# Kernel optimization log

Measured on AMD Instinct MI355X. Metric: run time of the kernel, lower is better.

The kernel has to match this reference:

```python
import jax, jax.numpy as jnp
import numpy as np

NUM_LEVELS = 16
RESOLUTIONS = np.array([16, 18, 20, 22, 25, 27, 30, 34, 38, 42, 47, 52, 58, 64, 72, 80], dtype=np.int32)
OFFSETS = np.concatenate([np.zeros(1, np.int64), np.cumsum(RESOLUTIONS.astype(np.int64) ** 3)]).astype(np.int32)
BATCH = 2
C_IN = 16
C_OUT = 16
K = 3


def setup_inputs() -> dict:
    key = jax.random.key(0)
    k1, k2, k3 = jax.random.split(key, 3)
    n_total = int(OFFSETS[-1])  # 1846083 embeddings across all levels
    inp = jax.random.normal(k1, (BATCH, n_total, C_IN), dtype=jnp.float32)
    weight = 0.1 * jax.random.normal(k2, (NUM_LEVELS, K, K, K, C_IN, C_OUT), dtype=jnp.float32)
    bias = 0.01 * jax.random.uniform(k3, (NUM_LEVELS, C_OUT), dtype=jnp.float32)
    # offsets / resolutions are static int buffers (kept as numpy so they stay
    # concrete under jit, mirroring registered int buffers in the torch module)
    return {"input": inp, "weight": weight, "bias": bias,
            "offsets": OFFSETS, "resolutions": RESOLUTIONS}


def _conv_all_levels(inp, weight, bias, offsets, resolutions):
    # inp: [B, N_total, C_in]; per level l the slice offsets[l]:offsets[l+1]
    # is a dense R_l^3 grid flattened x-fastest (idx = x + y*R + z*R^2).
    B = inp.shape[0]
    dn = ('NDHWC', 'DHWIO', 'NDHWC')
    outs = []
    for l in range(NUM_LEVELS):
        R = int(resolutions[l])
        off = int(offsets[l])
        x = inp[:, off:off + R ** 3, :].reshape(B, R, R, R, C_IN)  # [B,Z,Y,X,Cin]
        y = jax.lax.conv_general_dilated(
            x, weight[l], window_strides=(1, 1, 1), padding='SAME',
            dimension_numbers=dn)  # zero-padded 3x3x3 neighborhood gather
        y = y + bias[l]
        outs.append(y.reshape(B, R ** 3, C_OUT))
    return jnp.concatenate(outs, axis=1)  # [B, N_total, C_out]


def reference(input, weight, bias, offsets, resolutions):
    return _conv_all_levels(input, weight, bias, offsets, resolutions)
```

## Files before the change

kernel.cpp:

```cpp
#include <hip/hip_runtime.h>

#define NLVL 16
#define NTOT 1846083
#define NBLK 16140

typedef float  f32x4  __attribute__((ext_vector_type(4)));
typedef __bf16 bf16x8 __attribute__((ext_vector_type(8)));
typedef __bf16 bf16x4 __attribute__((ext_vector_type(4)));
typedef unsigned int u32x4 __attribute__((ext_vector_type(4)));

__constant__ int c_R[NLVL]      = {16,18,20,22,25,27,30,34,38,42,47,52,58,64,72,80};
__constant__ int c_off[NLVL]    = {0,4096,9928,17928,28576,44201,63884,90884,130188,185060,259148,362971,503579,698691,960835,1334083};
__constant__ int c_czy[NLVL]    = {4,5,5,6,7,7,8,9,10,11,12,13,15,16,18,20};
__constant__ int c_cx[NLVL]     = {1,2,2,2,2,2,2,3,3,3,3,4,4,4,5,5};
__constant__ int c_base[NLVL+1] = {0,32,132,232,376,572,768,1024,1510,2110,2836,3700,5052,6852,8900,12140,16140};

__device__ __align__(16) unsigned short g_bfrag[NLVL*14*64*8];

__global__ void prep_bfrag(const float* __restrict__ wgt) {
    int tid = blockIdx.x * 256 + threadIdx.x;
    if (tid >= NLVL*14*64) return;
    int lane = tid & 63;
    int p    = (tid >> 6) % 14;
    int l    = tid / (14*64);
    int quad = lane >> 4, co = lane & 15;
    unsigned short v[8];
#pragma unroll
    for (int j = 0; j < 8; ++j) {
        int k  = quad*8 + j;
        int t  = 2*p + (k >> 4);
        int ci = k & 15;
        float f = (t < 27) ? wgt[((l*27 + t)*16 + ci)*16 + co] : 0.f;
        v[j] = __builtin_bit_cast(unsigned short, (__bf16)f);
    }
    u32x4 pk;
    pk[0] = (unsigned)v[0] | ((unsigned)v[1] << 16);
    pk[1] = (unsigned)v[2] | ((unsigned)v[3] << 16);
    pk[2] = (unsigned)v[4] | ((unsigned)v[5] << 16);
    pk[3] = (unsigned)v[6] | ((unsigned)v[7] << 16);
    *(u32x4*)&g_bfrag[(size_t)tid*8] = pk;
}

__global__ void conv_kernel(const float* __restrict__ in,
                            const float* __restrict__ bias,
                            float* __restrict__ out) {
    __shared__ __align__(16) __bf16 slab[6*6*18*16];

    const int bid = blockIdx.x;
    int l = 0;
#pragma unroll
    for (int i = 1; i < NLVL; ++i) if (bid >= c_base[i]) l = i;
    const int R = c_R[l], off = c_off[l], czy = c_czy[l], cx = c_cx[l];

    int local = bid - c_base[l];
    int per_b = czy*czy*cx;
    int bb = local / per_b;       int r1 = local - bb*per_b;
    int zt = r1 / (czy*cx);       int r2 = r1 - zt*(czy*cx);
    int yt = r2 / cx;             int xt = r2 - yt*cx;
    const int z0 = zt*4, y0 = yt*4, x0 = xt*16;

    const int tid = threadIdx.x;
    for (int c = tid; c < 2592; c += 256) {
        int row = c / 72;  int pos = c - row*72;
        int zp = row / 6;  int yp  = row - zp*6;
        int xp = pos >> 2; int ci4 = (pos & 3) << 2;
        int z = z0 + zp - 1, y = y0 + yp - 1, x = x0 + xp - 1;
        f32x4 v = {0.f, 0.f, 0.f, 0.f};
        if ((unsigned)z < (unsigned)R && (unsigned)y < (unsigned)R && (unsigned)x < (unsigned)R) {
            long e = ((long)bb*NTOT + off + ((z*R + y)*R + x)) * 16 + ci4;
            v = *(const f32x4*)(in + e);
        }
        bf16x4 h = { (__bf16)v[0], (__bf16)v[1], (__bf16)v[2], (__bf16)v[3] };
        *(bf16x4*)&slab[(row*18 + xp)*16 + ci4] = h;
    }

    const int lane = tid & 63;
    const int wv   = tid >> 6;
    const int quad = lane >> 4;
    const int co   = lane & 15;
    const int m    = lane & 15;
    const int qh   = quad >> 1;
    bf16x8 bf[14];
#pragma unroll
    for (int p = 0; p < 14; ++p)
        bf[p] = *(const bf16x8*)&g_bfrag[(size_t)((l*14 + p)*64 + lane)*8];

    __syncthreads();

    f32x4 acc0 = {0,0,0,0}, acc1 = {0,0,0,0}, acc2 = {0,0,0,0}, acc3 = {0,0,0,0};
    const char* sb = (const char*)slab;
    const int abase = wv*576 + m*32 + (quad & 1)*16;
#pragma unroll
    for (int p = 0; p < 14; ++p) {
        const int t0 = 2*p;
        const int t1 = (2*p + 1 > 26) ? 26 : 2*p + 1;
        const int c0 = (t0/9)*3456 + ((t0%9)/3)*576 + (t0%3)*32;
        const int c1 = (t1/9)*3456 + ((t1%9)/3)*576 + (t1%3)*32;
        const char* ap = sb + abase + (qh ? c1 : c0);
        bf16x8 a0 = *(const bf16x8*)(ap);
        bf16x8 a1 = *(const bf16x8*)(ap + 3456);
        bf16x8 a2 = *(const bf16x8*)(ap + 2*3456);
        bf16x8 a3 = *(const bf16x8*)(ap + 3*3456);
        acc0 = __builtin_amdgcn_mfma_f32_16x16x32_bf16(a0, bf[p], acc0, 0, 0, 0);
        acc1 = __builtin_amdgcn_mfma_f32_16x16x32_bf16(a1, bf[p], acc1, 0, 0, 0);
        acc2 = __builtin_amdgcn_mfma_f32_16x16x32_bf16(a2, bf[p], acc2, 0, 0, 0);
        acc3 = __builtin_amdgcn_mfma_f32_16x16x32_bf16(a3, bf[p], acc3, 0, 0, 0);
    }

    const int yw = y0 + wv;
    if (yw >= R) return;
    const float bv = bias[(l << 4) + co];
    const long obase = (long)bb*NTOT + off;
    f32x4 accs[4] = {acc0, acc1, acc2, acc3};
#pragma unroll
    for (int zi = 0; zi < 4; ++zi) {
        int z = z0 + zi;
        if (z >= R) break;
        long rb = (obase + ((long)z*R + yw)*R) * 16 + co;
#pragma unroll
        for (int rr = 0; rr < 4; ++rr) {
            int x = x0 + quad*4 + rr;
            if (x < R) out[rb + (long)x*16] = accs[zi][rr] + bv;
        }
    }
}

extern "C" void kernel_launch(void* const* d_in, const int* in_sizes, int n_in,
                              void* d_out, int out_size, void* d_ws, size_t ws_size,
                              hipStream_t stream) {
    const float* inp = (const float*)d_in[0];
    const float* wgt = (const float*)d_in[1];
    const float* bia = (const float*)d_in[2];
    float* out = (float*)d_out;
    prep_bfrag<<<dim3(56), dim3(256), 0, stream>>>(wgt);
    conv_kernel<<<dim3(NBLK), dim3(256), 0, stream>>>(inp, bia, out);
}
```

Before: 508.5 us.

## Stream z-planes through double-buffered LDS with rolling accumulators per z-slab

Replaces the per-block 6x6x18 halo slab, which covered 4 z-planes, with a loop that streams one z-plane at a time through a double-buffered LDS slab. Each plane feeds three rolling accumulators, one per kernel depth, so the z-halo is loaded once per 16-plane column instead of re-read by every 4-plane tile. The weights are regrouped into three depth sets of five fragments each. Blocks are ordered largest level first and the grid shrinks to fewer, longer blocks with launch bounds set for occupancy. In exchange, each plane step costs a barrier, parallelism drops, and padding the 9 taps per depth to 10 adds some wasted MFMA work.

```diff
diff --git a/kernel.cpp b/kernel.cpp
--- a/kernel.cpp
+++ b/kernel.cpp
@@ -2,35 +2,37 @@
 
 #define NLVL 16
 #define NTOT 1846083
-#define NBLK 16140
+#define NBLK 4376
 
 typedef float  f32x4  __attribute__((ext_vector_type(4)));
 typedef __bf16 bf16x8 __attribute__((ext_vector_type(8)));
 typedef __bf16 bf16x4 __attribute__((ext_vector_type(4)));
 typedef unsigned int u32x4 __attribute__((ext_vector_type(4)));
 
-__constant__ int c_R[NLVL]      = {16,18,20,22,25,27,30,34,38,42,47,52,58,64,72,80};
-__constant__ int c_off[NLVL]    = {0,4096,9928,17928,28576,44201,63884,90884,130188,185060,259148,362971,503579,698691,960835,1334083};
-__constant__ int c_czy[NLVL]    = {4,5,5,6,7,7,8,9,10,11,12,13,15,16,18,20};
-__constant__ int c_cx[NLVL]     = {1,2,2,2,2,2,2,3,3,3,3,4,4,4,5,5};
-__constant__ int c_base[NLVL+1] = {0,32,132,232,376,572,768,1024,1510,2110,2836,3700,5052,6852,8900,12140,16140};
+__constant__ int c_R[NLVL]   = {16,18,20,22,25,27,30,34,38,42,47,52,58,64,72,80};
+__constant__ int c_off[NLVL] = {0,4096,9928,17928,28576,44201,63884,90884,130188,185060,259148,362971,503579,698691,960835,1334083};
+__constant__ int c_czy[NLVL] = {4,5,5,6,7,7,8,9,10,11,12,13,15,16,18,20};
+__constant__ int c_cx[NLVL]  = {1,2,2,2,2,2,2,3,3,3,3,4,4,4,5,5};
+__constant__ int c_base[17]  = {0,1000,1900,2412,2892,3308,3524,3722,3902,4064,4128,4184,4240,4288,4328,4368,4376};
 
-__device__ __align__(16) unsigned short g_bfrag[NLVL*14*64*8];
+__device__ __align__(16) unsigned short g_bfrag[NLVL*3*5*64*8];
 
 __global__ void prep_bfrag(const float* __restrict__ wgt) {
     int tid = blockIdx.x * 256 + threadIdx.x;
-    if (tid >= NLVL*14*64) return;
+    if (tid >= NLVL*3*5*64) return;
     int lane = tid & 63;
-    int p    = (tid >> 6) % 14;
-    int l    = tid / (14*64);
+    int p    = (tid >> 6) % 5;
+    int d    = (tid / (5*64)) % 3;
+    int l    = tid / (3*5*64);
     int quad = lane >> 4, co = lane & 15;
     unsigned short v[8];
 #pragma unroll
     for (int j = 0; j < 8; ++j) {
-        int k  = quad*8 + j;
-        int t  = 2*p + (k >> 4);
-        int ci = k & 15;
-        float f = (t < 27) ? wgt[((l*27 + t)*16 + ci)*16 + co] : 0.f;
+        int k   = quad*8 + j;
+        int tip = k >> 4;
+        int ci  = k & 15;
+        int t2  = 2*p + tip;
+        float f = (t2 < 9) ? wgt[((l*27 + d*9 + t2)*16 + ci)*16 + co] : 0.f;
         v[j] = __builtin_bit_cast(unsigned short, (__bf16)f);
     }
     u32x4 pk;
@@ -41,87 +43,142 @@
     *(u32x4*)&g_bfrag[(size_t)tid*8] = pk;
 }
 
-__global__ void conv_kernel(const float* __restrict__ in,
-                            const float* __restrict__ bias,
-                            float* __restrict__ out) {
-    __shared__ __align__(16) __bf16 slab[6*6*18*16];
+__global__ __launch_bounds__(256, 3)
+void conv_kernel(const float* __restrict__ in,
+                 const float* __restrict__ bias,
+                 float* __restrict__ out) {
+    __shared__ __align__(16) __bf16 slab[2*1728];
 
     const int bid = blockIdx.x;
-    int l = 0;
+    int idx = 0;
 #pragma unroll
-    for (int i = 1; i < NLVL; ++i) if (bid >= c_base[i]) l = i;
+    for (int i = 1; i < 16; ++i) if (bid >= c_base[i]) idx = i;
+    const int l = 15 - idx;
     const int R = c_R[l], off = c_off[l], czy = c_czy[l], cx = c_cx[l];
 
-    int local = bid - c_base[l];
-    int per_b = czy*czy*cx;
-    int bb = local / per_b;       int r1 = local - bb*per_b;
-    int zt = r1 / (czy*cx);       int r2 = r1 - zt*(czy*cx);
-    int yt = r2 / cx;             int xt = r2 - yt*cx;
-    const int z0 = zt*4, y0 = yt*4, x0 = xt*16;
+    int local = bid - c_base[idx];
+    int per_b = czy*cx*cx;
+    int bb = local / per_b;         int r1 = local - bb*per_b;
+    int zt = r1 / (czy*cx);         int r2 = r1 - zt*(czy*cx);
+    int yt = r2 / cx;               int xt = r2 - yt*cx;
+    const int z0 = zt*16;
+    const int z1 = (z0 + 16 < R) ? z0 + 16 : R;
+    const int y0 = yt*4, x0 = xt*16;
 
-    const int tid = threadIdx.x;
-    for (int c = tid; c < 2592; c += 256) {
-        int row = c / 72;  int pos = c - row*72;
-        int zp = row / 6;  int yp  = row - zp*6;
-        int xp = pos >> 2; int ci4 = (pos & 3) << 2;
-        int z = z0 + zp - 1, y = y0 + yp - 1, x = x0 + xp - 1;
-        f32x4 v = {0.f, 0.f, 0.f, 0.f};
-        if ((unsigned)z < (unsigned)R && (unsigned)y < (unsigned)R && (unsigned)x < (unsigned)R) {
-            long e = ((long)bb*NTOT + off + ((z*R + y)*R + x)) * 16 + ci4;
-            v = *(const f32x4*)(in + e);
-        }
-        bf16x4 h = { (__bf16)v[0], (__bf16)v[1], (__bf16)v[2], (__bf16)v[3] };
-        *(bf16x4*)&slab[(row*18 + xp)*16 + ci4] = h;
-    }
-
-    const int lane = tid & 63;
-    const int wv   = tid >> 6;
+    const int t    = threadIdx.x;
+    const int lane = t & 63;
+    const int wv   = t >> 6;
     const int quad = lane >> 4;
     const int co   = lane & 15;
     const int m    = lane & 15;
     const int qh   = quad >> 1;
-    bf16x8 bf[14];
+
+    bf16x8 bfr[15];
 #pragma unroll
-    for (int p = 0; p < 14; ++p)
-        bf[p] = *(const bf16x8*)&g_bfrag[(size_t)((l*14 + p)*64 + lane)*8];
+    for (int d = 0; d < 3; ++d)
+#pragma unroll
+        for (int p = 0; p < 5; ++p)
+            bfr[d*5+p] = *(const bf16x8*)&g_bfrag[(size_t)(((l*3 + d)*5 + p)*64 + lane)*8];
 
+    const int albase = wv*576 + m*32 + (quad & 1)*16;
+    int aoff[5];
+    {
+        const int T0[5] = {0, 64, 608, 1152, 1216};
+        const int T1[5] = {32, 576, 640, 1184, 1216};
+#pragma unroll
+        for (int p = 0; p < 5; ++p) aoff[p] = albase + (qh ? T1[p] : T0[p]);
+    }
+
+    const long zs = (long)R*R*16;
+    long g0 = 0, g1 = 0; int lo0 = 0, lo1 = 0; bool yx0 = false, yx1 = false;
+    {
+        int c = t;
+        int yp = c/72; int rem = c - yp*72; int xp = rem>>2; int ci4 = (rem&3)<<2;
+        lo0 = (yp*18 + xp)*16 + ci4;
+        int y = y0 + yp - 1, x = x0 + xp - 1;
+        yx0 = ((unsigned)y < (unsigned)R) && ((unsigned)x < (unsigned)R);
+        g0 = ((long)bb*NTOT + off)*16 + ((long)y*R + x)*16 + ci4;
+    }
+    const bool has1 = (t < 176);
+    if (has1) {
+        int c = t + 256;
+        int yp = c/72; int rem = c - yp*72; int xp = rem>>2; int ci4 = (rem&3)<<2;
+        lo1 = (yp*18 + xp)*16 + ci4;
+        int y = y0 + yp - 1, x = x0 + xp - 1;
+        yx1 = ((unsigned)y < (unsigned)R) && ((unsigned)x < (unsigned)R);
+        g1 = ((long)bb*NTOT + off)*16 + ((long)y*R + x)*16 + ci4;
+    }
+
+    __bf16* sbr = slab;
+    __bf16* sbw = slab + 1728;
+
+    {
+        int zn = z0 - 1;
+        bool zok = (unsigned)zn < (unsigned)R;
+        f32x4 v0 = {0,0,0,0}, v1 = {0,0,0,0};
+        if (zok && yx0) v0 = *(const f32x4*)(in + g0 + (long)zn*zs);
+        if (has1 && zok && yx1) v1 = *(const f32x4*)(in + g1 + (long)zn*zs);
+        bf16x4 h0 = {(__bf16)v0[0],(__bf16)v0[1],(__bf16)v0[2],(__bf16)v0[3]};
+        *(bf16x4*)(sbr + lo0) = h0;
+        if (has1) {
+            bf16x4 h1 = {(__bf16)v1[0],(__bf16)v1[1],(__bf16)v1[2],(__bf16)v1[3]};
+            *(bf16x4*)(sbr + lo1) = h1;
+        }
+    }
     __syncthreads();
 
-    f32x4 acc0 = {0,0,0,0}, acc1 = {0,0,0,0}, acc2 = {0,0,0,0}, acc3 = {0,0,0,0};
-    const char* sb = (const char*)slab;
-    const int abase = wv*576 + m*32 + (quad & 1)*16;
+    const bool ywok = (y0 + wv) < R;
+    const float bv = bias[(l << 4) + co];
+    const long obase = ((long)bb*NTOT + off)*16;
+
+    f32x4 accA = {0,0,0,0}, accB = {0,0,0,0}, accC = {0,0,0,0};
+    const int steps = z1 - z0 + 2;
+
+    for (int i = 0; i < steps; ++i) {
+        const int zp = z0 - 1 + i;
+        const int zn = zp + 1;
+        const bool sok = (zn <= z1);
+
+        f32x4 v0 = {0,0,0,0}, v1 = {0,0,0,0};
+        if (sok) {
+            bool zok = (unsigned)zn < (unsigned)R;
+            if (zok && yx0) v0 = *(const f32x4*)(in + g0 + (long)zn*zs);
+            if (has1 && zok && yx1) v1 = *(const f32x4*)(in + g1 + (long)zn*zs);
+        }
+
+        const char* sb = (const char*)sbr;
 #pragma unroll
-    for (int p = 0; p < 14; ++p) {
-        const int t0 = 2*p;
-        const int t1 = (2*p + 1 > 26) ? 26 : 2*p + 1;
-        const int c0 = (t0/9)*3456 + ((t0%9)/3)*576 + (t0%3)*32;
-        const int c1 = (t1/9)*3456 + ((t1%9)/3)*576 + (t1%3)*32;
-        const char* ap = sb + abase + (qh ? c1 : c0);
-        bf16x8 a0 = *(const bf16x8*)(ap);
-        bf16x8 a1 = *(const bf16x8*)(ap + 3456);
-        bf16x8 a2 = *(const bf16x8*)(ap + 2*3456);
-        bf16x8 a3 = *(const bf16x8*)(ap + 3*3456);
-        acc0 = __builtin_amdgcn_mfma_f32_16x16x32_bf16(a0, bf[p], acc0, 0, 0, 0);
-        acc1 = __builtin_amdgcn_mfma_f32_16x16x32_bf16(a1, bf[p], acc1, 0, 0, 0);
-        acc2 = __builtin_amdgcn_mfma_f32_16x16x32_bf16(a2, bf[p], acc2, 0, 0, 0);
-        acc3 = __builtin_amdgcn_mfma_f32_16x16x32_bf16(a3, bf[p], acc3, 0, 0, 0);
-    }
+        for (int p = 0; p < 5; ++p) {
+            bf16x8 a = *(const bf16x8*)(sb + aoff[p]);
+            accC = __builtin_amdgcn_mfma_f32_16x16x32_bf16(a, bfr[p],      accC, 0, 0, 0);
+            accB = __builtin_amdgcn_mfma_f32_16x16x32_bf16(a, bfr[5+p],  accB, 0, 0, 0);
+            accA = __builtin_amdgcn_mfma_f32_16x16x32_bf16(a, bfr[10+p], accA, 0, 0, 0);
+        }
 
-    const int yw = y0 + wv;
-    if (yw >= R) return;
-    const float bv = bias[(l << 4) + co];
-    const long obase = (long)bb*NTOT + off;
-    f32x4 accs[4] = {acc0, acc1, acc2, acc3};
+        if (sok) {
+            bf16x4 h0 = {(__bf16)v0[0],(__bf16)v0[1],(__bf16)v0[2],(__bf16)v0[3]};
+            *(bf16x4*)(sbw + lo0) = h0;
+            if (has1) {
+                bf16x4 h1 = {(__bf16)v1[0],(__bf16)v1[1],(__bf16)v1[2],(__bf16)v1[3]};
+                *(bf16x4*)(sbw + lo1) = h1;
+            }
+        }
+
+        if (i >= 2 && ywok) {
+            int z = zp - 1;
+            long rb = obase + (((long)z*R + (y0 + wv))*R)*16 + co;
 #pragma unroll
-    for (int zi = 0; zi < 4; ++zi) {
-        int z = z0 + zi;
-        if (z >= R) break;
-        long rb = (obase + ((long)z*R + yw)*R) * 16 + co;
-#pragma unroll
-        for (int rr = 0; rr < 4; ++rr) {
-            int x = x0 + quad*4 + rr;
-            if (x < R) out[rb + (long)x*16] = accs[zi][rr] + bv;
+            for (int rr = 0; rr < 4; ++rr) {
+                int x = x0 + quad*4 + rr;
+                if (x < R) out[rb + (long)x*16] = accA[rr] + bv;
+            }
         }
+
+        accA = accB; accB = accC;
+        accC = (f32x4){0,0,0,0};
+
+        __syncthreads();
+        __bf16* tmp = sbr; sbr = sbw; sbw = tmp;
     }
 }
 
@@ -132,6 +189,6 @@
     const float* wgt = (const float*)d_in[1];
     const float* bia = (const float*)d_in[2];
     float* out = (float*)d_out;
-    prep_bfrag<<<dim3(56), dim3(256), 0, stream>>>(wgt);
+    prep_bfrag<<<dim3((NLVL*3*5*64 + 255)/256), dim3(256), 0, stream>>>(wgt);
     conv_kernel<<<dim3(NBLK), dim3(256), 0, stream>>>(inp, bia, out);
 }
```

Result: faster. 440.3 us (-13.4%).
